# Kernel tuning notes

Hardware: AMD Instinct MI355X
Metric: run time of the kernel (lower is better)

## Reference

```python
import jax, jax.numpy as jnp
import numpy as np

B, C, H, W = 16, 256, 32, 32
K = 3          # kernel size
KK = K * K     # matrix_batch = 9 kernel positions
N = 256        # out_channels = n (power of 2, nstack = 1)


def setup_inputs() -> dict:
    key = jax.random.key(0)
    k1, k2, k3, k4 = jax.random.split(key, 4)
    s = 1.0 / np.sqrt(2.0)  # repo's 'regular' param init scale
    return {
        "x": jax.random.normal(k1, (B, C, H, W), jnp.float32),
        "twiddle1": jax.random.normal(k2, (KK, N - 1, 2, 2), jnp.float32) * s,
        "twiddle2": jax.random.normal(k3, (KK, N - 1, 2, 2), jnp.float32) * s,
        "bias": jax.random.normal(k4, (KK, N), jnp.float32) * 0.01,
    }


def _butterfly_tied(twiddle, x, increasing):
    """Tied-weight butterfly multiply.
    twiddle: (s, n-1, 2, 2); x: (b, s, n). At stride st, twiddle[:, st-1:2*st-1]
    (length st) is shared across the n/(2*st) blocks (matches butterfly_mult_torch).
    """
    b, s, n = x.shape
    m = n.bit_length() - 1  # log2(n)
    strides = [1 << i for i in range(m)]
    if not increasing:
        strides = strides[::-1]
    for st in strides:
        t = twiddle[:, st - 1:2 * st - 1]            # (s, st, 2, 2)
        xr = x.reshape(b, s, n // (2 * st), 2, st)   # (b, s, g, 2, st)
        # out[b,s,g,i,l] = sum_k t[s,l,i,k] * xr[b,s,g,k,l]
        x = jnp.einsum('slik,bsgkl->bsgil', t, xr).reshape(b, s, n)
    return x


def reference(x, twiddle1, twiddle2, bias):
    b, c, h, w = x.shape
    # im2col / F.unfold with kernel 3, pad 1, stride 1 -> (b, c, 9, h*w),
    # kernel positions in row-major order (matches torch unfold layout).
    xp = jnp.pad(x, ((0, 0), (0, 0), (1, 1), (1, 1)))
    patches = jnp.stack(
        [xp[:, :, i:i + h, j:j + w] for i in range(K) for j in range(K)], axis=2
    )  # (b, c, 9, h, w)
    inp = patches.reshape(b, c, KK, h * w).transpose(0, 3, 2, 1)
    inp = inp.reshape(b * h * w, KK, c)  # (batch*h*w, 9, c)
    # BB^T: B^T (decreasing stride) then B (increasing stride), bias on last.
    y = _butterfly_tied(twiddle1, inp, increasing=False)
    y = _butterfly_tied(twiddle2, y, increasing=True) + bias  # bias: (9, N)
    out = y.mean(axis=1)  # average over the 9 kernel positions -> (b*h*w, N)
    return out.reshape(b, h * w, N).transpose(0, 2, 1).reshape(b, N, h, w)
```

## Files before the change

kernel.cpp:

```cpp
#include <hip/hip_runtime.h>
#include <hip/hip_bf16.h>

typedef __attribute__((ext_vector_type(8))) short short8;
typedef __attribute__((ext_vector_type(4))) float float4v;
typedef __attribute__((ext_vector_type(16))) float float16v;

#define XT_BYTES (16*32*34*34*8*2)
#define WG_BYTES (9*4*4*8*64*8*2)

__global__ __launch_bounds__(256) void k_prep(const float* __restrict__ x,
                                              const float* __restrict__ tw1,
                                              const float* __restrict__ tw2,
                                              const float* __restrict__ bias,
                                              __hip_bfloat16* __restrict__ xTg,
                                              __hip_bfloat16* __restrict__ Wg,
                                              float* __restrict__ biasout) {
  __shared__ __align__(16) char smem[256 * 33 * 4];
  int blk = blockIdx.x;
  int tid = threadIdx.x;

  if (blk < 512) {
    float* tile = (float*)smem;
    char* xTB = (char*)xTg;
    int h = blk & 31, b = blk >> 5;
    {
      int w4 = (tid & 7) * 4, c0 = tid >> 3;
#pragma unroll
      for (int j = 0; j < 8; ++j) {
        int ci = c0 + 32 * j;
        float4 v = *(const float4*)&x[((b * 256 + ci) * 32 + h) * 32 + w4];
        *(float4*)&tile[ci * 33 + w4] = v;
      }
    }
    __syncthreads();
    {
      int g0 = tid >> 5, w = tid & 31;
#pragma unroll
      for (int gi = 0; gi < 4; ++gi) {
        int g = gi * 8 + g0;
        union { short8 s; __hip_bfloat16 hv[8]; } pk;
#pragma unroll
        for (int cc = 0; cc < 8; ++cc)
          pk.hv[cc] = __float2bfloat16(tile[(g * 8 + cc) * 33 + w]);
        *(short8*)(xTB + ((((b * 32 + g) * 34 + h + 1) * 34) + (w + 1)) * 16) = pk.s;
      }
    }
    if (h < 2) {
      uint4 z4 = {0u, 0u, 0u, 0u};
      int edge = h * 33;
      for (int i = tid; i < 32 * 34; i += 256) {
        int g = i / 34, w = i - g * 34;
        *(uint4*)(xTB + ((((b * 32 + g) * 34 + edge) * 34) + w) * 16) = z4;
      }
      for (int i = tid; i < 32 * 32; i += 256) {
        int g = i >> 5, hh = 1 + (i & 31);
        *(uint4*)(xTB + ((((b * 32 + g) * 34 + hh) * 34) + edge) * 16) = z4;
      }
    }
    return;
  }

  int wblk = blk - 512;
  if (wblk == 144) {
    if (tid < 256) {
      float a = 0.f;
#pragma unroll
      for (int s = 0; s < 9; ++s) a += bias[s * 256 + tid];
      biasout[tid] = a * (1.f / 9.f);
    }
    return;
  }
  float* mat = (float*)smem;
  float* tws = (float*)(smem + 17408);
  int sidx = wblk >> 4;
  int colbase = (wblk & 15) * 16;

  for (int i = tid; i < 255 * 4; i += 256) {
    tws[i]           = tw1[sidx * 255 * 4 + i];
    tws[255 * 4 + i] = tw2[sidx * 255 * 4 + i];
  }
  __syncthreads();

  int c  = tid >> 4;
  int rg = tid & 15;
  int cg = colbase + c;

  float xs[16];

#pragma unroll
  for (int j = 0; j < 16; ++j) xs[j] = (j * 16 + rg == cg) ? 1.f : 0.f;

#define SSTAGE_S(PH, ST, M)                                                   \
  {                                                                           \
    _Pragma("unroll")                                                         \
    for (int jb = 0; jb < 16; jb += 2 * (M)) {                                \
      _Pragma("unroll")                                                       \
      for (int q = 0; q < (M); ++q) {                                         \
        float4 tv = *(const float4*)&tws[((PH)*255 + (ST)-1 + q*16 + rg) * 4];\
        float x0 = xs[jb + q], x1 = xs[jb + q + (M)];                         \
        xs[jb + q]       = tv.x * x0 + tv.y * x1;                             \
        xs[jb + q + (M)] = tv.z * x0 + tv.w * x1;                             \
      }                                                                       \
    }                                                                         \
  }

#define RSTAGE(PH, ST)                                                        \
  {                                                                           \
    _Pragma("unroll")                                                         \
    for (int base = 0; base < 16; base += 2 * (ST)) {                         \
      _Pragma("unroll")                                                       \
      for (int q = 0; q < (ST); ++q) {                                        \
        float4 tv = *(const float4*)&tws[((PH) * 255 + (ST) - 1 + q) * 4];    \
        float x0 = xs[base + q], x1 = xs[base + q + (ST)];                    \
        xs[base + q]        = tv.x * x0 + tv.y * x1;                          \
        xs[base + q + (ST)] = tv.z * x0 + tv.w * x1;                          \
      }                                                                       \
    }                                                                         \
  }

  SSTAGE_S(0, 128, 8) SSTAGE_S(0, 64, 4) SSTAGE_S(0, 32, 2) SSTAGE_S(0, 16, 1)

  {
    float* mc = mat + c * 272;
#pragma unroll
    for (int j = 0; j < 16; ++j) mc[j * 17 + rg] = xs[j];
  }
  __syncthreads();
  {
    float* mc = mat + c * 272;
#pragma unroll
    for (int j = 0; j < 16; ++j) xs[j] = mc[rg * 17 + j];
  }

  RSTAGE(0, 8) RSTAGE(0, 4) RSTAGE(0, 2) RSTAGE(0, 1)
  RSTAGE(1, 1) RSTAGE(1, 2) RSTAGE(1, 4) RSTAGE(1, 8)

  {
    float* mc = mat + c * 272;
#pragma unroll
    for (int j = 0; j < 16; ++j) mc[rg * 17 + j] = xs[j];
  }
  __syncthreads();
  {
    float* mc = mat + c * 272;
#pragma unroll
    for (int j = 0; j < 16; ++j) xs[j] = mc[j * 17 + rg];
  }

  SSTAGE_S(1, 16, 1) SSTAGE_S(1, 32, 2) SSTAGE_S(1, 64, 4) SSTAGE_S(1, 128, 8)

  {
    int pr = cg >> 6, g = (cg >> 3) & 7, c8 = cg & 7;
#pragma unroll
    for (int j = 0; j < 16; ++j) {
      int nq = j >> 2, nl = (j & 3) * 16 + rg;
      int o = ((((sidx * 4 + pr) * 4 + nq) * 8 + g) * 64 + nl) * 8 + c8;
      Wg[o] = __float2bfloat16(xs[j] * (1.f / 9.f));
    }
  }
#undef SSTAGE_S
#undef RSTAGE
}

__global__ __launch_bounds__(256, 4) void k_gemm(const __hip_bfloat16* __restrict__ xTg,
                                                 const __hip_bfloat16* __restrict__ Wg,
                                                 const float* __restrict__ biasout,
                                                 float* __restrict__ out) {
  __shared__ __align__(64) char lds[32768];
  const char* WgB = (const char*)Wg;
  const char* xTB = (const char*)xTg;

  int blk  = blockIdx.x;
  int rest = blk >> 3;
  int b    = 2 * (blk & 7) + (rest >> 6);
  int r2   = rest & 63;
  int nq   = r2 & 3;
  int pt   = r2 >> 2;
  int h0   = pt * 2;

  int tid  = threadIdx.x;
  int lane = tid & 63;
  int wk   = tid >> 6;
  int half = lane >> 5;
  int l31  = lane & 31;

  float16v acc[2][2];
#pragma unroll
  for (int mt = 0; mt < 2; ++mt)
#pragma unroll
    for (int p2 = 0; p2 < 2; ++p2)
#pragma unroll
      for (int e = 0; e < 16; ++e) acc[mt][p2][e] = 0.f;

  int aoff = ((2 * wk + half) * 64 + l31) * 16;
  int bbase = ((((b * 32 + 2 * wk + half) * 34 + h0) * 34) + l31) * 16;

#pragma unroll 2
  for (int p = 0; p < 4; ++p) {
    const char* Bp = xTB + bbase + p * (8 * 34 * 34) * 16;
    const char* Ap = WgB + (p * 4 + nq) * 8192;
#pragma unroll
    for (int si = 0; si < 3; ++si) {
#pragma unroll
      for (int sj = 0; sj < 3; ++sj) {
        const char* Aslab = Ap + (si * 3 + sj) * (16 * 8192);
        short8 a0 = *(const short8*)(Aslab + aoff);
        short8 a1 = *(const short8*)(Aslab + aoff + 32 * 16);
        const char* Bq = Bp + (si * 34 + sj) * 16;
        short8 b0 = *(const short8*)(Bq);
        short8 b1 = *(const short8*)(Bq + 34 * 16);
        acc[0][0] = __builtin_amdgcn_mfma_f32_32x32x16_bf16(a0, b0, acc[0][0], 0, 0, 0);
        acc[0][1] = __builtin_amdgcn_mfma_f32_32x32x16_bf16(a0, b1, acc[0][1], 0, 0, 0);
        acc[1][0] = __builtin_amdgcn_mfma_f32_32x32x16_bf16(a1, b0, acc[1][0], 0, 0, 0);
        acc[1][1] = __builtin_amdgcn_mfma_f32_32x32x16_bf16(a1, b1, acc[1][1], 0, 0, 0);
      }
    }
  }

  float bv[16];
  if (wk < 2) {
#pragma unroll
    for (int reg = 0; reg < 16; ++reg)
      bv[reg] = biasout[nq * 64 + wk * 32 + (reg & 3) + 8 * (reg >> 2) + 4 * half];
  }

  auto st16 = [&](int slot, const float16v& v) {
    char* base = lds + slot * 4096 + lane * 16;
    *(float4v*)(base)        = (float4v){v[0],  v[1],  v[2],  v[3]};
    *(float4v*)(base + 1024) = (float4v){v[4],  v[5],  v[6],  v[7]};
    *(float4v*)(base + 2048) = (float4v){v[8],  v[9],  v[10], v[11]};
    *(float4v*)(base + 3072) = (float4v){v[12], v[13], v[14], v[15]};
  };
  auto ld16add = [&](int slot, float16v& v) {
    const char* base = lds + slot * 4096 + lane * 16;
    float4v t0 = *(const float4v*)(base);
    float4v t1 = *(const float4v*)(base + 1024);
    float4v t2 = *(const float4v*)(base + 2048);
    float4v t3 = *(const float4v*)(base + 3072);
    v[0] += t0[0]; v[1] += t0[1]; v[2]  += t0[2]; v[3]  += t0[3];
    v[4] += t1[0]; v[5] += t1[1]; v[6]  += t1[2]; v[7]  += t1[3];
    v[8] += t2[0]; v[9] += t2[1]; v[10] += t2[2]; v[11] += t2[3];
    v[12] += t3[0]; v[13] += t3[1]; v[14] += t3[2]; v[15] += t3[3];
  };

  __syncthreads();
  if (wk == 2) { st16(0, acc[0][0]); st16(1, acc[0][1]); st16(2, acc[1][0]); st16(3, acc[1][1]); }
  if (wk == 3) { st16(4, acc[0][0]); st16(5, acc[0][1]); st16(6, acc[1][0]); st16(7, acc[1][1]); }
  __syncthreads();
  if (wk == 0) { ld16add(0, acc[0][0]); ld16add(1, acc[0][1]); ld16add(2, acc[1][0]); ld16add(3, acc[1][1]); }
  if (wk == 1) { ld16add(4, acc[0][0]); ld16add(5, acc[0][1]); ld16add(6, acc[1][0]); ld16add(7, acc[1][1]); }
  __syncthreads();
  if (wk == 1) { st16(0, acc[0][0]); st16(1, acc[0][1]); }
  if (wk == 0) { st16(4, acc[1][0]); st16(5, acc[1][1]); }
  __syncthreads();
  if (wk == 0) {
    ld16add(0, acc[0][0]); ld16add(1, acc[0][1]);
#pragma unroll
    for (int reg = 0; reg < 16; ++reg) {
      int n = nq * 64 + (reg & 3) + 8 * (reg >> 2) + 4 * half;
      float* o0 = &out[((b * 256 + n) * 32 + h0) * 32 + l31];
      o0[0]  = acc[0][0][reg] + bv[reg];
      o0[32] = acc[0][1][reg] + bv[reg];
    }
  }
  if (wk == 1) {
    ld16add(4, acc[1][0]); ld16add(5, acc[1][1]);
#pragma unroll
    for (int reg = 0; reg < 16; ++reg) {
      int n = nq * 64 + 32 + (reg & 3) + 8 * (reg >> 2) + 4 * half;
      float* o0 = &out[((b * 256 + n) * 32 + h0) * 32 + l31];
      o0[0]  = acc[1][0][reg] + bv[reg];
      o0[32] = acc[1][1][reg] + bv[reg];
    }
  }
}

extern "C" void kernel_launch(void* const* d_in, const int* in_sizes, int n_in,
                              void* d_out, int out_size, void* d_ws, size_t ws_size,
                              hipStream_t stream) {
  const float* x    = (const float*)d_in[0];
  const float* tw1  = (const float*)d_in[1];
  const float* tw2  = (const float*)d_in[2];
  const float* bias = (const float*)d_in[3];
  float* out = (float*)d_out;

  char* ws = (char*)d_ws;
  __hip_bfloat16* xTg = (__hip_bfloat16*)ws;
  __hip_bfloat16* Wg  = (__hip_bfloat16*)(ws + XT_BYTES);
  float* biasout      = (float*)(ws + XT_BYTES + WG_BYTES);

  k_prep<<<657, 256, 0, stream>>>(x, tw1, tw2, bias, xTg, Wg, biasout);
  k_gemm<<<1024, 256, 0, stream>>>(xTg, Wg, biasout, out);
}
```

Baseline: 102.5 us.

## Stage input halo tiles in LDS and split waves over output channels

The GEMM kernel now copies the input halo tile for each half of the channel range into LDS with a cooperative load. Each wave then reads its B operands from LDS and owns a distinct 32-channel slice of outputs across the full reduction. Previously each wave read B straight from global memory and partial sums were combined through an LDS reduction. The new layout removes that cross-wave reduction, halves the grid to 512 blocks with 128 output channels per block, and lowers the occupancy hint. The cost is extra barriers and a serialized copy-then-compute phase per stage.

```diff
diff --git a/kernel.cpp b/kernel.cpp
--- a/kernel.cpp
+++ b/kernel.cpp
@@ -2,7 +2,6 @@
 #include <hip/hip_bf16.h>
 
 typedef __attribute__((ext_vector_type(8))) short short8;
-typedef __attribute__((ext_vector_type(4))) float float4v;
 typedef __attribute__((ext_vector_type(16))) float float16v;
 
 #define XT_BYTES (16*32*34*34*8*2)
@@ -162,116 +161,79 @@
 #undef RSTAGE
 }
 
-__global__ __launch_bounds__(256, 4) void k_gemm(const __hip_bfloat16* __restrict__ xTg,
+__global__ __launch_bounds__(256, 2) void k_gemm(const __hip_bfloat16* __restrict__ xTg,
                                                  const __hip_bfloat16* __restrict__ Wg,
                                                  const float* __restrict__ biasout,
                                                  float* __restrict__ out) {
-  __shared__ __align__(64) char lds[32768];
+  __shared__ __align__(128) char lds[34816];
   const char* WgB = (const char*)Wg;
   const char* xTB = (const char*)xTg;
 
   int blk  = blockIdx.x;
   int rest = blk >> 3;
-  int b    = 2 * (blk & 7) + (rest >> 6);
-  int r2   = rest & 63;
-  int nq   = r2 & 3;
-  int pt   = r2 >> 2;
+  int b    = 2 * (blk & 7) + (rest >> 5);
+  int r2   = rest & 31;
+  int pt   = r2 >> 1;
+  int nh   = r2 & 1;
   int h0   = pt * 2;
 
   int tid  = threadIdx.x;
   int lane = tid & 63;
-  int wk   = tid >> 6;
+  int w    = tid >> 6;
   int half = lane >> 5;
   int l31  = lane & 31;
 
-  float16v acc[2][2];
-#pragma unroll
-  for (int mt = 0; mt < 2; ++mt)
-#pragma unroll
-    for (int p2 = 0; p2 < 2; ++p2)
-#pragma unroll
-      for (int e = 0; e < 16; ++e) acc[mt][p2][e] = 0.f;
-
-  int aoff = ((2 * wk + half) * 64 + l31) * 16;
-  int bbase = ((((b * 32 + 2 * wk + half) * 34 + h0) * 34) + l31) * 16;
-
-#pragma unroll 2
-  for (int p = 0; p < 4; ++p) {
-    const char* Bp = xTB + bbase + p * (8 * 34 * 34) * 16;
-    const char* Ap = WgB + (p * 4 + nq) * 8192;
+  int w8   = nh * 4 + w;
+  int nq   = w8 >> 1;
+  int noff = (w8 & 1) * 32;
+
+  float16v acc[2];
+#pragma unroll
+  for (int p2 = 0; p2 < 2; ++p2)
+#pragma unroll
+    for (int e = 0; e < 16; ++e) acc[p2][e] = 0.f;
+
+  const char* pA = WgB + nq * 8192 + (noff + l31) * 16;
+
+#pragma unroll 1
+  for (int st = 0; st < 2; ++st) {
+    __syncthreads();
+    for (int c = tid; c < 2176; c += 256) {
+      int g   = c / 136;
+      int rem = c - g * 136;
+      int r   = rem / 34;
+      int col = rem - r * 34;
+      short8 v = *(const short8*)(xTB + (b * 32 + st * 16 + g) * 18496 +
+                                  (h0 + r) * 544 + col * 16);
+      *(short8*)(lds + c * 16) = v;
+    }
+    __syncthreads();
 #pragma unroll
     for (int si = 0; si < 3; ++si) {
 #pragma unroll
       for (int sj = 0; sj < 3; ++sj) {
-        const char* Aslab = Ap + (si * 3 + sj) * (16 * 8192);
-        short8 a0 = *(const short8*)(Aslab + aoff);
-        short8 a1 = *(const short8*)(Aslab + aoff + 32 * 16);
-        const char* Bq = Bp + (si * 34 + sj) * 16;
-        short8 b0 = *(const short8*)(Bq);
-        short8 b1 = *(const short8*)(Bq + 34 * 16);
-        acc[0][0] = __builtin_amdgcn_mfma_f32_32x32x16_bf16(a0, b0, acc[0][0], 0, 0, 0);
-        acc[0][1] = __builtin_amdgcn_mfma_f32_32x32x16_bf16(a0, b1, acc[0][1], 0, 0, 0);
-        acc[1][0] = __builtin_amdgcn_mfma_f32_32x32x16_bf16(a1, b0, acc[1][0], 0, 0, 0);
-        acc[1][1] = __builtin_amdgcn_mfma_f32_32x32x16_bf16(a1, b1, acc[1][1], 0, 0, 0);
-      }
-    }
-  }
-
-  float bv[16];
-  if (wk < 2) {
-#pragma unroll
-    for (int reg = 0; reg < 16; ++reg)
-      bv[reg] = biasout[nq * 64 + wk * 32 + (reg & 3) + 8 * (reg >> 2) + 4 * half];
-  }
-
-  auto st16 = [&](int slot, const float16v& v) {
-    char* base = lds + slot * 4096 + lane * 16;
-    *(float4v*)(base)        = (float4v){v[0],  v[1],  v[2],  v[3]};
-    *(float4v*)(base + 1024) = (float4v){v[4],  v[5],  v[6],  v[7]};
-    *(float4v*)(base + 2048) = (float4v){v[8],  v[9],  v[10], v[11]};
-    *(float4v*)(base + 3072) = (float4v){v[12], v[13], v[14], v[15]};
-  };
-  auto ld16add = [&](int slot, float16v& v) {
-    const char* base = lds + slot * 4096 + lane * 16;
-    float4v t0 = *(const float4v*)(base);
-    float4v t1 = *(const float4v*)(base + 1024);
-    float4v t2 = *(const float4v*)(base + 2048);
-    float4v t3 = *(const float4v*)(base + 3072);
-    v[0] += t0[0]; v[1] += t0[1]; v[2]  += t0[2]; v[3]  += t0[3];
-    v[4] += t1[0]; v[5] += t1[1]; v[6]  += t1[2]; v[7]  += t1[3];
-    v[8] += t2[0]; v[9] += t2[1]; v[10] += t2[2]; v[11] += t2[3];
-    v[12] += t3[0]; v[13] += t3[1]; v[14] += t3[2]; v[15] += t3[3];
-  };
-
-  __syncthreads();
-  if (wk == 2) { st16(0, acc[0][0]); st16(1, acc[0][1]); st16(2, acc[1][0]); st16(3, acc[1][1]); }
-  if (wk == 3) { st16(4, acc[0][0]); st16(5, acc[0][1]); st16(6, acc[1][0]); st16(7, acc[1][1]); }
-  __syncthreads();
-  if (wk == 0) { ld16add(0, acc[0][0]); ld16add(1, acc[0][1]); ld16add(2, acc[1][0]); ld16add(3, acc[1][1]); }
-  if (wk == 1) { ld16add(4, acc[0][0]); ld16add(5, acc[0][1]); ld16add(6, acc[1][0]); ld16add(7, acc[1][1]); }
-  __syncthreads();
-  if (wk == 1) { st16(0, acc[0][0]); st16(1, acc[0][1]); }
-  if (wk == 0) { st16(4, acc[1][0]); st16(5, acc[1][1]); }
-  __syncthreads();
-  if (wk == 0) {
-    ld16add(0, acc[0][0]); ld16add(1, acc[0][1]);
-#pragma unroll
-    for (int reg = 0; reg < 16; ++reg) {
-      int n = nq * 64 + (reg & 3) + 8 * (reg >> 2) + 4 * half;
-      float* o0 = &out[((b * 256 + n) * 32 + h0) * 32 + l31];
-      o0[0]  = acc[0][0][reg] + bv[reg];
-      o0[32] = acc[0][1][reg] + bv[reg];
-    }
-  }
-  if (wk == 1) {
-    ld16add(4, acc[1][0]); ld16add(5, acc[1][1]);
-#pragma unroll
-    for (int reg = 0; reg < 16; ++reg) {
-      int n = nq * 64 + 32 + (reg & 3) + 8 * (reg >> 2) + 4 * half;
-      float* o0 = &out[((b * 256 + n) * 32 + h0) * 32 + l31];
-      o0[0]  = acc[1][0][reg] + bv[reg];
-      o0[32] = acc[1][1][reg] + bv[reg];
-    }
+#pragma unroll
+        for (int t = 0; t < 8; ++t) {
+          const short8 a = *(const short8*)(pA +
+              (si * 3 + sj) * 131072 + (st * 2 + (t >> 2)) * 32768 +
+              ((2 * t + half) & 7) * 1024);
+          const char* bb = lds + (((2 * t + half) * 4 + si) * 34 + sj + l31) * 16;
+          short8 b0 = *(const short8*)(bb);
+          short8 b1 = *(const short8*)(bb + 544);
+          acc[0] = __builtin_amdgcn_mfma_f32_32x32x16_bf16(a, b0, acc[0], 0, 0, 0);
+          acc[1] = __builtin_amdgcn_mfma_f32_32x32x16_bf16(a, b1, acc[1], 0, 0, 0);
+        }
+      }
+    }
+  }
+
+#pragma unroll
+  for (int reg = 0; reg < 16; ++reg) {
+    int n = nh * 128 + w * 32 + (reg & 3) + 8 * (reg >> 2) + 4 * half;
+    float bv = biasout[n];
+    float* o0 = &out[((b * 256 + n) * 32 + h0) * 32 + l31];
+    o0[0]  = acc[0][reg] + bv;
+    o0[32] = acc[1][reg] + bv;
   }
 }
 
@@ -290,5 +252,5 @@
   float* biasout      = (float*)(ws + XT_BYTES + WG_BYTES);
 
   k_prep<<<657, 256, 0, stream>>>(x, tw1, tw2, bias, xTg, Wg, biasout);
-  k_gemm<<<1024, 256, 0, stream>>>(xTg, Wg, biasout, out);
+  k_gemm<<<512, 256, 0, stream>>>(xTg, Wg, biasout, out);
 }
```

After: 113.5 us. 10.7% more time.
